# Optimization experiments

Hardware: AMD Instinct MI355X
Metric: run time of the kernel (lower is better)

## Reference

```python
import jax, jax.numpy as jnp
import numpy as np

N = 1024      # num_nodes
D = 64        # node_embedding_dim
H = 64        # hidden_dim
LN_EPS = 1e-5


def setup_inputs() -> dict:
    key = jax.random.key(0)
    ks = jax.random.split(key, 6)
    node_embeddings = jax.random.normal(ks[0], (N, D), dtype=jnp.float32)
    valid_mask = jax.random.randint(ks[1], (N * N,), 0, 2).astype(jnp.float32)
    s1 = 1.0 / np.sqrt(2 * D)
    s2 = 1.0 / np.sqrt(H)
    W1 = jax.random.normal(ks[2], (2 * D, H), dtype=jnp.float32) * s1
    b1 = jnp.zeros((H,), jnp.float32)
    g1 = jnp.ones((H,), jnp.float32)
    be1 = jnp.zeros((H,), jnp.float32)
    W2 = jax.random.normal(ks[3], (H, H), dtype=jnp.float32) * s2
    b2 = jnp.zeros((H,), jnp.float32)
    g2 = jnp.ones((H,), jnp.float32)
    be2 = jnp.zeros((H,), jnp.float32)
    W3 = jax.random.normal(ks[4], (H, 1), dtype=jnp.float32) * s2
    b3 = jnp.zeros((1,), jnp.float32)
    return {
        "node_embeddings": node_embeddings, "valid_mask": valid_mask,
        "W1": W1, "b1": b1, "g1": g1, "be1": be1,
        "W2": W2, "b2": b2, "g2": g2, "be2": be2,
        "W3": W3, "b3": b3,
    }


def _layer_norm(x, g, b):
    m = jnp.mean(x, axis=-1, keepdims=True)
    v = jnp.mean((x - m) ** 2, axis=-1, keepdims=True)
    return (x - m) * jax.lax.rsqrt(v + LN_EPS) * g + b


def reference(node_embeddings, valid_mask, W1, b1, g1, be1, W2, b2, g2, be2, W3, b3):
    n, d = node_embeddings.shape
    # Build all ordered pairs (i, j): concat([emb_i, emb_j]) -> [n*n, 2d]
    src = jnp.broadcast_to(node_embeddings[:, None, :], (n, n, d))
    tgt = jnp.broadcast_to(node_embeddings[None, :, :], (n, n, d))
    e = jnp.concatenate([src, tgt], axis=-1).reshape(n * n, 2 * d)
    # MLP: Linear -> LayerNorm -> ReLU (x2 hidden) -> Linear(1)
    h = jax.nn.relu(_layer_norm(e @ W1 + b1, g1, be1))
    h = jax.nn.relu(_layer_norm(h @ W2 + b2, g2, be2))
    scores = (h @ W3 + b3)[:, 0]  # [n*n]
    # Original never scores self-edges (i == j) and multiplies by valid_mask.
    off_diag = 1.0 - jnp.eye(n, dtype=scores.dtype).reshape(-1)
    return scores * valid_mask * off_diag
```

## Files before the change

### kernel.cpp

```cpp
#include <hip/hip_runtime.h>
#include <hip/hip_bf16.h>

#define NN 1024
#define LN_EPS 1e-5f

typedef __bf16 bf16x8 __attribute__((ext_vector_type(8)));
typedef float floatx4 __attribute__((ext_vector_type(4)));
typedef float floatx2 __attribute__((ext_vector_type(2)));

__device__ __forceinline__ floatx4 splat4(float s) { return (floatx4){s, s, s, s}; }

__global__ void precompute_ab(const float* __restrict__ emb, const float* __restrict__ W1,
                              const float* __restrict__ b1, const float* __restrict__ W2,
                              float* __restrict__ Ap, float* __restrict__ Bt4,
                              __bf16* __restrict__ Abf, __bf16* __restrict__ Bbf,
                              float* __restrict__ sumA, float* __restrict__ sumB,
                              float* __restrict__ sumA2, float* __restrict__ sumB2,
                              __bf16* __restrict__ Wf) {
    if (blockIdx.x == 1024) {
        int lane = threadIdx.x;
        int m_l = lane & 15, kg = lane >> 4;
#pragma unroll
        for (int mt = 0; mt < 4; mt++)
#pragma unroll
            for (int kc = 0; kc < 2; kc++) {
                bf16x8 f;
#pragma unroll
                for (int t = 0; t < 8; t++) {
                    int k = kc * 32 + kg * 8 + t;
                    f[t] = (__bf16)W2[k * 64 + mt * 16 + m_l];
                }
                *(bf16x8*)&Wf[((mt * 2 + kc) * 64 + lane) * 8] = f;
            }
        return;
    }
    __shared__ __align__(16) float e[64];
    int i = blockIdx.x, h = threadIdx.x;
    e[h] = emb[i * 64 + h];
    __syncthreads();
    float a = b1[h], b = 0.f;
#pragma unroll
    for (int d = 0; d < 64; d++) {
        a = fmaf(e[d], W1[d * 64 + h], a);
        b = fmaf(e[d], W1[(64 + d) * 64 + h], b);
    }
    Ap[i * 64 + h] = a;
    Abf[i * 64 + h] = (__bf16)a;
    Bt4[(h >> 2) * 4096 + i * 4 + (h & 3)] = b;
    Bbf[i * 64 + h] = (__bf16)b;
    float ra = a, rb = b, ra2 = a * a, rb2 = b * b;
#pragma unroll
    for (int off = 1; off < 64; off <<= 1) {
        ra += __shfl_xor(ra, off);
        rb += __shfl_xor(rb, off);
        ra2 += __shfl_xor(ra2, off);
        rb2 += __shfl_xor(rb2, off);
    }
    if (h == 0) { sumA[i] = ra; sumB[i] = rb; sumA2[i] = ra2; sumB2[i] = rb2; }
}

__global__ __launch_bounds__(256, 4) void fused(
    const float* __restrict__ Ap, const float* __restrict__ Bt4,
    const __bf16* __restrict__ Abf, const __bf16* __restrict__ Bbf,
    const __bf16* __restrict__ Wf,
    const float* __restrict__ sumA, const float* __restrict__ sumB,
    const float* __restrict__ sumA2, const float* __restrict__ sumB2,
    const float* __restrict__ g1, const float* __restrict__ be1, const float* __restrict__ b2,
    const float* __restrict__ g2, const float* __restrict__ be2, const float* __restrict__ W3,
    const float* __restrict__ b3, const float* __restrict__ mask, float* __restrict__ out) {
    __shared__ __align__(16) float Arow[64], G1[64], BE1[64], B2s[64], G2s[64], BE2s[64], W3s[64];
    __shared__ __align__(16) __bf16 h1t[4][64 * 64];

    int tid = threadIdx.x;
    int wave = tid >> 6, lane = tid & 63;
    int i = blockIdx.x >> 2;
    int j0 = (blockIdx.x & 3) * 256 + wave * 64;

    if (tid < 64) {
        Arow[tid] = Ap[i * 64 + tid];
        G1[tid] = g1[tid];  BE1[tid] = be1[tid];
        B2s[tid] = b2[tid]; G2s[tid] = g2[tid]; BE2s[tid] = be2[tid];
        W3s[tid] = W3[tid];
    }
    __syncthreads();

    int m_l = lane & 15, kg = lane >> 4;

    bf16x8 afA0 = *(const bf16x8*)&Abf[i * 64 + kg * 8];
    bf16x8 afA1 = *(const bf16x8*)&Abf[i * 64 + 32 + kg * 8];
    floatx4 xacc[4];
#pragma unroll
    for (int nt = 0; nt < 4; nt++) xacc[nt] = splat4(0.f);
#pragma unroll
    for (int nt = 0; nt < 4; nt++) {
        const __bf16* bp = &Bbf[(j0 + nt * 16 + m_l) * 64 + kg * 8];
        xacc[nt] = __builtin_amdgcn_mfma_f32_16x16x32_bf16(afA0, *(const bf16x8*)bp, xacc[nt], 0, 0, 0);
        xacc[nt] = __builtin_amdgcn_mfma_f32_16x16x32_bf16(afA1, *(const bf16x8*)(bp + 32), xacc[nt], 0, 0, 0);
    }
    float c0 = (kg & 2) ? xacc[2][0] : xacc[0][0];
    float c1 = (kg & 2) ? xacc[3][0] : xacc[1][0];
    float cross = (kg & 1) ? c1 : c0;

    float m1 = (sumA[i] + sumB[j0 + lane]) * 0.015625f;
    float sq = fmaf(2.f, cross, sumA2[i] + sumB2[j0 + lane]);
    float var1 = fmaf(m1, -m1, sq * 0.015625f);
    float rs1 = rsqrtf(var1 + LN_EPS);
    floatx4 RS = splat4(rs1), OF = splat4(-m1 * rs1);

    bf16x8 afrag[4][2];
#pragma unroll
    for (int mt = 0; mt < 4; mt++)
#pragma unroll
        for (int kc = 0; kc < 2; kc++)
            afrag[mt][kc] = *(const bf16x8*)&Wf[((mt * 2 + kc) * 64 + lane) * 8];

    __bf16* rowp = &h1t[wave][lane * 64];
    int sw = lane & 7;
    const float* btp = Bt4 + (j0 + lane) * 4;
#pragma unroll
    for (int c = 0; c < 8; c++) {
        floatx4 bb0 = *(const floatx4*)(btp + (2 * c) * 4096);
        floatx4 bb1 = *(const floatx4*)(btp + (2 * c + 1) * 4096);
        floatx4 a0 = *(const floatx4*)&Arow[c * 8];
        floatx4 a1 = *(const floatx4*)&Arow[c * 8 + 4];
        floatx4 gg0 = *(const floatx4*)&G1[c * 8];
        floatx4 gg1 = *(const floatx4*)&G1[c * 8 + 4];
        floatx4 ee0 = *(const floatx4*)&BE1[c * 8];
        floatx4 ee1 = *(const floatx4*)&BE1[c * 8 + 4];
        floatx4 y0 = ((a0 + bb0) * RS + OF) * gg0 + ee0;
        floatx4 y1 = ((a1 + bb1) * RS + OF) * gg1 + ee1;
        y0 = __builtin_elementwise_max(y0, splat4(0.f));
        y1 = __builtin_elementwise_max(y1, splat4(0.f));
        bf16x8 fr;
        fr[0] = (__bf16)y0[0]; fr[1] = (__bf16)y0[1]; fr[2] = (__bf16)y0[2]; fr[3] = (__bf16)y0[3];
        fr[4] = (__bf16)y1[0]; fr[5] = (__bf16)y1[1]; fr[6] = (__bf16)y1[2]; fr[7] = (__bf16)y1[3];
        *(bf16x8*)(rowp + ((c ^ sw) * 8)) = fr;
    }
    asm volatile("s_waitcnt lgkmcnt(0)" ::: "memory");

    floatx4 b2r[4];
#pragma unroll
    for (int mt = 0; mt < 4; mt++) b2r[mt] = *(const floatx4*)&B2s[mt * 16 + kg * 4];
    floatx4 acc[4][4];
#pragma unroll
    for (int mt = 0; mt < 4; mt++)
#pragma unroll
        for (int nt = 0; nt < 4; nt++) acc[mt][nt] = b2r[mt];

    const __bf16* wbase = &h1t[wave][0];
#pragma unroll
    for (int nt = 0; nt < 4; nt++) {
        int pair = nt * 16 + m_l;
#pragma unroll
        for (int kc = 0; kc < 2; kc++) {
            int chunk = kc * 4 + kg;
            bf16x8 bfrag = *(const bf16x8*)(wbase + pair * 64 + ((chunk ^ (pair & 7)) * 8));
#pragma unroll
            for (int mt = 0; mt < 4; mt++)
                acc[mt][nt] =
                    __builtin_amdgcn_mfma_f32_16x16x32_bf16(afrag[mt][kc], bfrag, acc[mt][nt], 0, 0, 0);
        }
    }

    floatx4 g2r[4], e2r[4], w3r[4];
#pragma unroll
    for (int mt = 0; mt < 4; mt++) {
        g2r[mt] = *(const floatx4*)&G2s[mt * 16 + kg * 4];
        e2r[mt] = *(const floatx4*)&BE2s[mt * 16 + kg * 4];
        w3r[mt] = *(const floatx4*)&W3s[mt * 16 + kg * 4];
    }
    float b3v = b3[0];

#pragma unroll
    for (int nt = 0; nt < 4; nt++) {
        floatx2 s2v = {0.f, 0.f}, q2v = {0.f, 0.f};
#pragma unroll
        for (int mt = 0; mt < 4; mt++) {
            floatx2 vlo = {acc[mt][nt][0], acc[mt][nt][1]};
            floatx2 vhi = {acc[mt][nt][2], acc[mt][nt][3]};
            s2v += vlo; s2v += vhi;
            q2v += vlo * vlo; q2v += vhi * vhi;
        }
        float s2 = s2v[0] + s2v[1];
        float q2 = q2v[0] + q2v[1];
        s2 += __shfl_xor(s2, 16); s2 += __shfl_xor(s2, 32);
        q2 += __shfl_xor(q2, 16); q2 += __shfl_xor(q2, 32);
        float m2 = s2 * 0.015625f;
        float rs2 = rsqrtf(fmaf(m2, -m2, q2 * 0.015625f) + LN_EPS);
        floatx2 P2 = {rs2, rs2};
        float o2s = -m2 * rs2;
        floatx2 O2 = {o2s, o2s};

        floatx2 scv = {0.f, 0.f};
#pragma unroll
        for (int mt = 0; mt < 4; mt++) {
#pragma unroll
            for (int hh = 0; hh < 2; hh++) {
                floatx2 v = {acc[mt][nt][2 * hh], acc[mt][nt][2 * hh + 1]};
                floatx2 g = {g2r[mt][2 * hh], g2r[mt][2 * hh + 1]};
                floatx2 e = {e2r[mt][2 * hh], e2r[mt][2 * hh + 1]};
                floatx2 w = {w3r[mt][2 * hh], w3r[mt][2 * hh + 1]};
                floatx2 y = (v * P2 + O2) * g + e;
                y = __builtin_elementwise_max(y, (floatx2){0.f, 0.f});
                scv += y * w;
            }
        }
        float sc = scv[0] + scv[1];
        sc += __shfl_xor(sc, 16); sc += __shfl_xor(sc, 32);

        if (kg == 0) {
            int j = j0 + nt * 16 + m_l;
            int p = i * NN + j;
            out[p] = (i == j) ? 0.f : (sc + b3v) * mask[p];
        }
    }
}

extern "C" void kernel_launch(void* const* d_in, const int* in_sizes, int n_in,
                              void* d_out, int out_size, void* d_ws, size_t ws_size,
                              hipStream_t stream) {
    const float* emb = (const float*)d_in[0];
    const float* mask = (const float*)d_in[1];
    const float* W1 = (const float*)d_in[2];
    const float* b1 = (const float*)d_in[3];
    const float* g1 = (const float*)d_in[4];
    const float* be1 = (const float*)d_in[5];
    const float* W2 = (const float*)d_in[6];
    const float* b2 = (const float*)d_in[7];
    const float* g2 = (const float*)d_in[8];
    const float* be2 = (const float*)d_in[9];
    const float* W3 = (const float*)d_in[10];
    const float* b3 = (const float*)d_in[11];
    float* out = (float*)d_out;

    float* Ap = (float*)d_ws;
    float* Bt4 = Ap + 65536;
    float* sA = Bt4 + 65536;
    float* sB = sA + 1024;
    float* sA2 = sB + 1024;
    float* sB2 = sA2 + 1024;
    __bf16* Abf = (__bf16*)(sB2 + 1024);
    __bf16* Bbf = Abf + 65536;
    __bf16* Wf = Bbf + 65536;

    precompute_ab<<<1025, 64, 0, stream>>>(emb, W1, b1, W2, Ap, Bt4, Abf, Bbf, sA, sB, sA2, sB2, Wf);
    fused<<<4096, 256, 0, stream>>>(Ap, Bt4, Abf, Bbf, Wf, sA, sB, sA2, sB2,
                                    g1, be1, b2, g2, be2, W3, b3, mask, out);
}
```

Before: 119.7 us.

## Compute LN1 variance directly and derive LN2 mean from precomputed W2 row sums

```diff
diff --git a/kernel.cpp b/kernel.cpp
--- a/kernel.cpp
+++ b/kernel.cpp
@@ -10,65 +10,71 @@
 
 __device__ __forceinline__ floatx4 splat4(float s) { return (floatx4){s, s, s, s}; }
 
-__global__ void precompute_ab(const float* __restrict__ emb, const float* __restrict__ W1,
-                              const float* __restrict__ b1, const float* __restrict__ W2,
-                              float* __restrict__ Ap, float* __restrict__ Bt4,
-                              __bf16* __restrict__ Abf, __bf16* __restrict__ Bbf,
-                              float* __restrict__ sumA, float* __restrict__ sumB,
-                              float* __restrict__ sumA2, float* __restrict__ sumB2,
-                              __bf16* __restrict__ Wf) {
-    if (blockIdx.x == 1024) {
-        int lane = threadIdx.x;
-        int m_l = lane & 15, kg = lane >> 4;
-#pragma unroll
-        for (int mt = 0; mt < 4; mt++)
-#pragma unroll
-            for (int kc = 0; kc < 2; kc++) {
-                bf16x8 f;
-#pragma unroll
-                for (int t = 0; t < 8; t++) {
-                    int k = kc * 32 + kg * 8 + t;
-                    f[t] = (__bf16)W2[k * 64 + mt * 16 + m_l];
+__global__ __launch_bounds__(256) void precompute_ab(
+    const float* __restrict__ emb, const float* __restrict__ W1,
+    const float* __restrict__ b1, const float* __restrict__ W2, const float* __restrict__ b2,
+    float* __restrict__ Ap, float* __restrict__ Bt4,
+    float* __restrict__ sumA, float* __restrict__ sumB,
+    float* __restrict__ Wc, float* __restrict__ sb2, __bf16* __restrict__ Wf) {
+    int tid = threadIdx.x, wv = tid >> 6, lane = tid & 63;
+    if (blockIdx.x == 256) {
+        if (wv == 0) {
+            int m_l = lane & 15, kg = lane >> 4;
+#pragma unroll
+            for (int mt = 0; mt < 4; mt++)
+#pragma unroll
+                for (int kc = 0; kc < 2; kc++) {
+                    bf16x8 f;
+#pragma unroll
+                    for (int t = 0; t < 8; t++) {
+                        int k = kc * 32 + kg * 8 + t;
+                        f[t] = (__bf16)W2[k * 64 + mt * 16 + m_l];
+                    }
+                    *(bf16x8*)&Wf[((mt * 2 + kc) * 64 + lane) * 8] = f;
                 }
-                *(bf16x8*)&Wf[((mt * 2 + kc) * 64 + lane) * 8] = f;
-            }
+        } else if (wv == 1) {
+            float s = 0.f;
+#pragma unroll
+            for (int h = 0; h < 64; h++) s += W2[lane * 64 + h];
+            Wc[lane] = s;
+        } else if (wv == 2) {
+            float v = b2[lane];
+#pragma unroll
+            for (int off = 1; off < 64; off <<= 1) v += __shfl_xor(v, off);
+            if (lane == 0) sb2[0] = v;
+        }
         return;
     }
-    __shared__ __align__(16) float e[64];
-    int i = blockIdx.x, h = threadIdx.x;
-    e[h] = emb[i * 64 + h];
+    __shared__ __align__(16) float e[4][64];
+    int i = blockIdx.x * 4 + wv, h = lane;
+    e[wv][h] = emb[i * 64 + h];
     __syncthreads();
     float a = b1[h], b = 0.f;
 #pragma unroll
     for (int d = 0; d < 64; d++) {
-        a = fmaf(e[d], W1[d * 64 + h], a);
-        b = fmaf(e[d], W1[(64 + d) * 64 + h], b);
+        a = fmaf(e[wv][d], W1[d * 64 + h], a);
+        b = fmaf(e[wv][d], W1[(64 + d) * 64 + h], b);
     }
     Ap[i * 64 + h] = a;
-    Abf[i * 64 + h] = (__bf16)a;
     Bt4[(h >> 2) * 4096 + i * 4 + (h & 3)] = b;
-    Bbf[i * 64 + h] = (__bf16)b;
-    float ra = a, rb = b, ra2 = a * a, rb2 = b * b;
+    float ra = a, rb = b;
 #pragma unroll
     for (int off = 1; off < 64; off <<= 1) {
         ra += __shfl_xor(ra, off);
         rb += __shfl_xor(rb, off);
-        ra2 += __shfl_xor(ra2, off);
-        rb2 += __shfl_xor(rb2, off);
-    }
-    if (h == 0) { sumA[i] = ra; sumB[i] = rb; sumA2[i] = ra2; sumB2[i] = rb2; }
+    }
+    if (h == 0) { sumA[i] = ra; sumB[i] = rb; }
 }
 
 __global__ __launch_bounds__(256, 4) void fused(
-    const float* __restrict__ Ap, const float* __restrict__ Bt4,
-    const __bf16* __restrict__ Abf, const __bf16* __restrict__ Bbf,
-    const __bf16* __restrict__ Wf,
+    const float* __restrict__ Ap, const float* __restrict__ Bt4, const __bf16* __restrict__ Wf,
     const float* __restrict__ sumA, const float* __restrict__ sumB,
-    const float* __restrict__ sumA2, const float* __restrict__ sumB2,
+    const float* __restrict__ Wcp, const float* __restrict__ sb2p,
     const float* __restrict__ g1, const float* __restrict__ be1, const float* __restrict__ b2,
     const float* __restrict__ g2, const float* __restrict__ be2, const float* __restrict__ W3,
     const float* __restrict__ b3, const float* __restrict__ mask, float* __restrict__ out) {
-    __shared__ __align__(16) float Arow[64], G1[64], BE1[64], B2s[64], G2s[64], BE2s[64], W3s[64];
+    __shared__ __align__(16) float Arow[64], G1[64], BE1[64], B2s[64], G2s[64], BE2s[64],
+        W3s[64], WCs[64];
     __shared__ __align__(16) __bf16 h1t[4][64 * 64];
 
     int tid = threadIdx.x;
@@ -80,62 +86,60 @@
         Arow[tid] = Ap[i * 64 + tid];
         G1[tid] = g1[tid];  BE1[tid] = be1[tid];
         B2s[tid] = b2[tid]; G2s[tid] = g2[tid]; BE2s[tid] = be2[tid];
-        W3s[tid] = W3[tid];
+        W3s[tid] = W3[tid]; WCs[tid] = Wcp[tid];
     }
     __syncthreads();
 
     int m_l = lane & 15, kg = lane >> 4;
 
-    bf16x8 afA0 = *(const bf16x8*)&Abf[i * 64 + kg * 8];
-    bf16x8 afA1 = *(const bf16x8*)&Abf[i * 64 + 32 + kg * 8];
-    floatx4 xacc[4];
-#pragma unroll
-    for (int nt = 0; nt < 4; nt++) xacc[nt] = splat4(0.f);
-#pragma unroll
-    for (int nt = 0; nt < 4; nt++) {
-        const __bf16* bp = &Bbf[(j0 + nt * 16 + m_l) * 64 + kg * 8];
-        xacc[nt] = __builtin_amdgcn_mfma_f32_16x16x32_bf16(afA0, *(const bf16x8*)bp, xacc[nt], 0, 0, 0);
-        xacc[nt] = __builtin_amdgcn_mfma_f32_16x16x32_bf16(afA1, *(const bf16x8*)(bp + 32), xacc[nt], 0, 0, 0);
-    }
-    float c0 = (kg & 2) ? xacc[2][0] : xacc[0][0];
-    float c1 = (kg & 2) ? xacc[3][0] : xacc[1][0];
-    float cross = (kg & 1) ? c1 : c0;
-
-    float m1 = (sumA[i] + sumB[j0 + lane]) * 0.015625f;
-    float sq = fmaf(2.f, cross, sumA2[i] + sumB2[j0 + lane]);
-    float var1 = fmaf(m1, -m1, sq * 0.015625f);
-    float rs1 = rsqrtf(var1 + LN_EPS);
+    float sBj = sumB[j0 + lane];
+    const float* btp = Bt4 + (j0 + lane) * 4;
+    floatx4 xs[16];
+    floatx4 qA = splat4(0.f), qB = splat4(0.f);
+#pragma unroll
+    for (int g = 0; g < 16; g++) {
+        floatx4 bb = *(const floatx4*)(btp + g * 4096);
+        floatx4 aa = *(const floatx4*)&Arow[g * 4];
+        floatx4 v = aa + bb;
+        xs[g] = v;
+        if (g & 1) qB += v * v;
+        else       qA += v * v;
+    }
+    floatx4 qs = qA + qB;
+    float sq = (qs[0] + qs[1]) + (qs[2] + qs[3]);
+    float m1 = (sumA[i] + sBj) * 0.015625f;
+    float rs1 = rsqrtf(fmaf(m1, -m1, sq * 0.015625f) + LN_EPS);
     floatx4 RS = splat4(rs1), OF = splat4(-m1 * rs1);
-
-    bf16x8 afrag[4][2];
-#pragma unroll
-    for (int mt = 0; mt < 4; mt++)
-#pragma unroll
-        for (int kc = 0; kc < 2; kc++)
-            afrag[mt][kc] = *(const bf16x8*)&Wf[((mt * 2 + kc) * 64 + lane) * 8];
 
     __bf16* rowp = &h1t[wave][lane * 64];
     int sw = lane & 7;
-    const float* btp = Bt4 + (j0 + lane) * 4;
+    floatx4 s2acc = splat4(0.f);
 #pragma unroll
     for (int c = 0; c < 8; c++) {
-        floatx4 bb0 = *(const floatx4*)(btp + (2 * c) * 4096);
-        floatx4 bb1 = *(const floatx4*)(btp + (2 * c + 1) * 4096);
-        floatx4 a0 = *(const floatx4*)&Arow[c * 8];
-        floatx4 a1 = *(const floatx4*)&Arow[c * 8 + 4];
         floatx4 gg0 = *(const floatx4*)&G1[c * 8];
         floatx4 gg1 = *(const floatx4*)&G1[c * 8 + 4];
         floatx4 ee0 = *(const floatx4*)&BE1[c * 8];
         floatx4 ee1 = *(const floatx4*)&BE1[c * 8 + 4];
-        floatx4 y0 = ((a0 + bb0) * RS + OF) * gg0 + ee0;
-        floatx4 y1 = ((a1 + bb1) * RS + OF) * gg1 + ee1;
+        floatx4 y0 = (xs[2 * c] * RS + OF) * gg0 + ee0;
+        floatx4 y1 = (xs[2 * c + 1] * RS + OF) * gg1 + ee1;
         y0 = __builtin_elementwise_max(y0, splat4(0.f));
         y1 = __builtin_elementwise_max(y1, splat4(0.f));
+        s2acc = y0 * (*(const floatx4*)&WCs[c * 8]) + s2acc;
+        s2acc = y1 * (*(const floatx4*)&WCs[c * 8 + 4]) + s2acc;
         bf16x8 fr;
         fr[0] = (__bf16)y0[0]; fr[1] = (__bf16)y0[1]; fr[2] = (__bf16)y0[2]; fr[3] = (__bf16)y0[3];
         fr[4] = (__bf16)y1[0]; fr[5] = (__bf16)y1[1]; fr[6] = (__bf16)y1[2]; fr[7] = (__bf16)y1[3];
         *(bf16x8*)(rowp + ((c ^ sw) * 8)) = fr;
     }
+    float s2p = ((s2acc[0] + s2acc[1]) + (s2acc[2] + s2acc[3])) + sb2p[0];
+
+    bf16x8 afrag[4][2];
+#pragma unroll
+    for (int mt = 0; mt < 4; mt++)
+#pragma unroll
+        for (int kc = 0; kc < 2; kc++)
+            afrag[mt][kc] = *(const bf16x8*)&Wf[((mt * 2 + kc) * 64 + lane) * 8];
+
     asm volatile("s_waitcnt lgkmcnt(0)" ::: "memory");
 
     floatx4 b2r[4];
@@ -173,17 +177,16 @@
 
 #pragma unroll
     for (int nt = 0; nt < 4; nt++) {
-        floatx2 s2v = {0.f, 0.f}, q2v = {0.f, 0.f};
+        float s2 = __shfl(s2p, nt * 16 + m_l);
+        floatx2 q2v = {0.f, 0.f};
 #pragma unroll
         for (int mt = 0; mt < 4; mt++) {
             floatx2 vlo = {acc[mt][nt][0], acc[mt][nt][1]};
             floatx2 vhi = {acc[mt][nt][2], acc[mt][nt][3]};
-            s2v += vlo; s2v += vhi;
-            q2v += vlo * vlo; q2v += vhi * vhi;
-        }
-        float s2 = s2v[0] + s2v[1];
+            q2v += vlo * vlo;
+            q2v += vhi * vhi;
+        }
         float q2 = q2v[0] + q2v[1];
-        s2 += __shfl_xor(s2, 16); s2 += __shfl_xor(s2, 32);
         q2 += __shfl_xor(q2, 16); q2 += __shfl_xor(q2, 32);
         float m2 = s2 * 0.015625f;
         float rs2 = rsqrtf(fmaf(m2, -m2, q2 * 0.015625f) + LN_EPS);
@@ -237,13 +240,11 @@
     float* Bt4 = Ap + 65536;
     float* sA = Bt4 + 65536;
     float* sB = sA + 1024;
-    float* sA2 = sB + 1024;
-    float* sB2 = sA2 + 1024;
-    __bf16* Abf = (__bf16*)(sB2 + 1024);
-    __bf16* Bbf = Abf + 65536;
-    __bf16* Wf = Bbf + 65536;
-
-    precompute_ab<<<1025, 64, 0, stream>>>(emb, W1, b1, W2, Ap, Bt4, Abf, Bbf, sA, sB, sA2, sB2, Wf);
-    fused<<<4096, 256, 0, stream>>>(Ap, Bt4, Abf, Bbf, Wf, sA, sB, sA2, sB2,
+    float* Wc = sB + 1024;
+    float* sb2 = Wc + 64;
+    __bf16* Wf = (__bf16*)(sb2 + 64);
+
+    precompute_ab<<<257, 256, 0, stream>>>(emb, W1, b1, W2, b2, Ap, Bt4, sA, sB, Wc, sb2, Wf);
+    fused<<<4096, 256, 0, stream>>>(Ap, Bt4, Wf, sA, sB, Wc, sb2,
                                     g1, be1, b2, g2, be2, W3, b3, mask, out);
 }
```

Result: no change. 120.1 us (+0.3%).
